# Kernel optimization log

Measured on AMD Instinct MI355X. Metric: run time of the kernel, lower is better.

## Reference

```python
import jax, jax.numpy as jnp
import numpy as np

B, H, F = 4096, 32, 1024     # batch, hp_num, feat_dim
N_CAT, CAT_DIM = 8, 16       # categorical dims 0..7, each |domain| = 16
N_CONT = H - N_CAT
LN_EPS = 1e-5


def setup_inputs() -> dict:
    key = jax.random.key(0)
    ks = jax.random.split(key, 8)
    s = 1.0 / np.sqrt(F)  # ~xavier scale
    return {
        "z": jax.random.normal(ks[0], (B, F), jnp.float32),
        "edge": jax.random.randint(ks[1], (2, 10), 0, B),
        # stacked per-hp projection Linears (weights stored as [in, out])
        "W_proj": jax.random.normal(ks[2], (H, F, F), jnp.float32) * s,
        "b_proj": jnp.zeros((H, F), jnp.float32),
        # LayerNorm over [hp_num, feat_dim]
        "ln_w": jnp.ones((H, F), jnp.float32),
        "ln_b": jnp.zeros((H, F), jnp.float32),
        # reverse_embedding for categorical dims (softmax heads)
        "W_cat": jax.random.normal(ks[3], (N_CAT, F, CAT_DIM), jnp.float32) * s,
        "b_cat": jnp.zeros((N_CAT, CAT_DIM), jnp.float32),
        # reverse_embedding for continuous dims (scalar heads)
        "W_cont": jax.random.normal(ks[4], (N_CONT, F, 1), jnp.float32) * s,
        "b_cont": jnp.zeros((N_CONT, 1), jnp.float32),
    }


def reference(z, edge, W_proj, b_proj, ln_w, ln_b, W_cat, b_cat, W_cont, b_cont):
    # per-hp projection: batched GEMM replacing batch*hp_num tiny Linears
    latent = jnp.einsum('bf,hfd->bhd', z, W_proj) + b_proj  # [B, H, F]
    # LayerNorm normalized over the last two dims [hp_num, feat_dim]
    mu = latent.mean(axis=(1, 2), keepdims=True)
    var = latent.var(axis=(1, 2), keepdims=True)
    latent = (latent - mu) * jax.lax.rsqrt(var + LN_EPS) * ln_w + ln_b
    latent = jax.nn.relu(latent)
    # reverse embeddings: categorical heads (dims 0..N_CAT-1) get softmax
    cat_logits = jnp.einsum('bhf,hfc->bhc', latent[:, :N_CAT], W_cat) + b_cat
    pred_cat = jax.nn.softmax(cat_logits, axis=-1)          # [B, N_CAT, CAT_DIM]
    pred_cont = jnp.einsum('bhf,hfc->bhc', latent[:, N_CAT:], W_cont) + b_cont  # [B, N_CONT, 1]
    return pred_cat, pred_cont, latent
```

## Files before the change

### kernel.cpp

```cpp
#include <hip/hip_runtime.h>

typedef unsigned short u16;
typedef __bf16 bf16x8 __attribute__((ext_vector_type(8)));
typedef float f32x4 __attribute__((ext_vector_type(4)));

#define B_SZ   4096
#define H_NUM  32
#define F_DIM  1024
#define NTOT   (H_NUM * F_DIM)
#define N_CAT  8
#define CAT_D  16
#define N_CONT 24
#define LN_EPS 1e-5f
#define NSTRIP 128

__device__ __forceinline__ u16 f2bf(float f) {
    unsigned int u = __builtin_bit_cast(unsigned int, f);
    unsigned int r = (u + 0x7FFFu + ((u >> 16) & 1u)) >> 16;
    return (u16)r;
}

__device__ __forceinline__ float bf2f(u16 v) {
    unsigned int u = ((unsigned int)v) << 16;
    return __builtin_bit_cast(float, u);
}

__device__ __forceinline__ void gl2lds16(const void* g, void* l) {
    __builtin_amdgcn_global_load_lds(
        (const __attribute__((address_space(1))) void*)g,
        (__attribute__((address_space(3))) void*)l,
        16, 0, 0);
}

__device__ __forceinline__ float wave_sum(float v) {
#pragma unroll
    for (int o = 32; o; o >>= 1) v += __shfl_xor(v, o);
    return v;
}

__global__ __launch_bounds__(256) void zconv(const float* __restrict__ z,
                                             u16* __restrict__ zb) {
    int i = blockIdx.x * 256 + threadIdx.x;
    float4 v = ((const float4*)z)[i];
    ushort4 o;
    o.x = f2bf(v.x); o.y = f2bf(v.y); o.z = f2bf(v.z); o.w = f2bf(v.w);
    ((ushort4*)zb)[i] = o;
}

__global__ __launch_bounds__(256) void transpose_w(const float* __restrict__ W,
                                                   u16* __restrict__ Wt) {
    __shared__ u16 tile[64][72];
    const int h = blockIdx.z;
    const int f0 = blockIdx.x * 64;
    const int d0 = blockIdx.y * 64;
    const float* Wh = W + (size_t)h * F_DIM * F_DIM;
    u16* Wth = Wt + (size_t)h * F_DIM * F_DIM;
    const int t = threadIdx.x;

#pragma unroll
    for (int i = 0; i < 4; ++i) {
        int idx = i * 256 + t;
        int fr = idx >> 4;
        int c4 = idx & 15;
        float4 v = *(const float4*)(Wh + (size_t)(f0 + fr) * F_DIM + d0 + c4 * 4);
        tile[fr][c4 * 4 + 0] = f2bf(v.x);
        tile[fr][c4 * 4 + 1] = f2bf(v.y);
        tile[fr][c4 * 4 + 2] = f2bf(v.z);
        tile[fr][c4 * 4 + 3] = f2bf(v.w);
    }
    __syncthreads();
#pragma unroll
    for (int i = 0; i < 2; ++i) {
        int idx = i * 256 + t;
        int dr = idx >> 3;
        int c8 = idx & 7;
        __attribute__((aligned(16))) u16 tmp[8];
#pragma unroll
        for (int j = 0; j < 8; ++j) tmp[j] = tile[c8 * 8 + j][dr];
        *(uint4*)(Wth + (size_t)(d0 + dr) * F_DIM + f0 + c8 * 8) = *(const uint4*)tmp;
    }
}

template <int BF>
__global__ __launch_bounds__(512, 2) void gemm256(const u16* __restrict__ A,
                                                  const u16* __restrict__ Bt,
                                                  const float* __restrict__ bproj,
                                                  u16* __restrict__ lat16,
                                                  float* __restrict__ latf,
                                                  float* __restrict__ psum,
                                                  float* __restrict__ psumsq) {
    extern __shared__ u16 dynlds[];
    const int t = threadIdx.x;
    const int wid = t >> 6;
    const int lane = t & 63;
    const int l16 = lane & 15;
    const int lk = lane >> 4;
    const int wm = wid >> 2;
    const int wn = wid & 3;

    const int wg = blockIdx.x;
    const int xcd = wg & 7;
    const int local = wg >> 3;
    const int m0 = (local & 15) * 256;
    const int n0 = ((xcd << 4) + (local >> 4)) * 256;

    f32x4 acc[8][4];
    const f32x4 zero = {0.f, 0.f, 0.f, 0.f};
#pragma unroll
    for (int m = 0; m < 8; ++m)
#pragma unroll
        for (int n = 0; n < 4; ++n) acc[m][n] = zero;

    auto stage = [&](int p, int ktn, int bn) {
        const char* srcbase = (p < 2) ? (const char*)A : (const char*)Bt;
        const int rowbase = (p < 2) ? (m0 + p * 128) : (n0 + (p - 2) * 128);
        u16* ldsbase = dynlds + bn * 32768 + (p >> 1) * 16384 + (p & 1) * 8192;
#pragma unroll
        for (int i = 0; i < 2; ++i) {
            int oo = i * 8192 + t * 16;
            int oos = oo ^ (((oo >> 7) & 7) << 4);
            int row = oo >> 7;
            int colb = oos & 127;
            gl2lds16(srcbase + (size_t)(rowbase + row) * 2048 + ktn * 128 + colb,
                     ldsbase + i * 4096 + (wid << 9));
        }
    };

#pragma unroll
    for (int p = 0; p < 4; ++p) stage(p, 0, 0);
    __syncthreads();

    const int swz = (l16 & 7) << 4;
    for (int kt = 0; kt < 16; ++kt) {
        const int buf = kt & 1;
        const char* aB = (const char*)(dynlds + buf * 32768 + wm * 8192);
        const char* bB = (const char*)(dynlds + buf * 32768 + 16384 + (wn >> 1) * 8192);
        bf16x8 bfr[4][2];
#pragma unroll
        for (int p = 0; p < 4; ++p) {
            if (kt < 15) stage(p, kt + 1, buf ^ 1);
            if (p == 0) {
#pragma unroll
                for (int nr = 0; nr < 4; ++nr)
#pragma unroll
                    for (int kk = 0; kk < 2; ++kk)
                        bfr[nr][kk] = *(const bf16x8*)(bB +
                            ((wn & 1) * 64 + nr * 16 + l16) * 128 +
                            ((kk * 64 + lk * 16) ^ swz));
            }
            bf16x8 afr[2][2];
#pragma unroll
            for (int mr = 0; mr < 2; ++mr)
#pragma unroll
                for (int kk = 0; kk < 2; ++kk)
                    afr[mr][kk] = *(const bf16x8*)(aB +
                        (p * 32 + mr * 16 + l16) * 128 +
                        ((kk * 64 + lk * 16) ^ swz));
            __builtin_amdgcn_s_setprio(1);
#pragma unroll
            for (int kk = 0; kk < 2; ++kk)
#pragma unroll
                for (int mr = 0; mr < 2; ++mr)
#pragma unroll
                    for (int nr = 0; nr < 4; ++nr)
                        acc[p * 2 + mr][nr] = __builtin_amdgcn_mfma_f32_16x16x32_bf16(
                            afr[mr][kk], bfr[nr][kk], acc[p * 2 + mr][nr], 0, 0, 0);
            __builtin_amdgcn_s_setprio(0);
        }
        __syncthreads();
    }

    float bias[4];
#pragma unroll
    for (int nr = 0; nr < 4; ++nr) bias[nr] = bproj[n0 + wn * 64 + nr * 16 + l16];

    float sm[8][4], s2[8][4];
#pragma unroll
    for (int mr = 0; mr < 8; ++mr)
#pragma unroll
        for (int j = 0; j < 4; ++j) { sm[mr][j] = 0.f; s2[mr][j] = 0.f; }

#pragma unroll
    for (int mr = 0; mr < 8; ++mr) {
#pragma unroll
        for (int j = 0; j < 4; ++j) {
            const int rowg = m0 + wm * 128 + mr * 16 + lk * 4 + j;
            size_t off = (size_t)rowg * NTOT + n0 + wn * 64 + l16;
#pragma unroll
            for (int nr = 0; nr < 4; ++nr) {
                float v = acc[mr][nr][j] + bias[nr];
                if (BF) lat16[off + nr * 16] = f2bf(v);
                else    latf[off + nr * 16] = v;
                sm[mr][j] += v;
                s2[mr][j] += v * v;
            }
        }
    }
#pragma unroll
    for (int o = 1; o < 16; o <<= 1) {
#pragma unroll
        for (int mr = 0; mr < 8; ++mr)
#pragma unroll
            for (int j = 0; j < 4; ++j) {
                sm[mr][j] += __shfl_xor(sm[mr][j], o);
                s2[mr][j] += __shfl_xor(s2[mr][j], o);
            }
    }
    float* sredf = (float*)dynlds;
    float* s2f   = sredf + 1024;
    __syncthreads();
    if (l16 == 0) {
#pragma unroll
        for (int mr = 0; mr < 8; ++mr)
#pragma unroll
            for (int j = 0; j < 4; ++j) {
                int r = wm * 128 + mr * 16 + lk * 4 + j;
                sredf[wn * 256 + r] = sm[mr][j];
                s2f[wn * 256 + r] = s2[mr][j];
            }
    }
    __syncthreads();
    if (t < 256) {
        const int strip = n0 >> 8;
        float S = sredf[t] + sredf[256 + t] + sredf[512 + t] + sredf[768 + t];
        float S2 = s2f[t] + s2f[256 + t] + s2f[512 + t] + s2f[768 + t];
        psum[(size_t)strip * B_SZ + m0 + t] = S;
        psumsq[(size_t)strip * B_SZ + m0 + t] = S2;
    }
}

__global__ __launch_bounds__(256) void ln_finalize(const float* __restrict__ psum,
                                                   const float* __restrict__ psumsq,
                                                   float* __restrict__ murs) {
    const int t = threadIdx.x;
    const int b0 = blockIdx.x * 64;
    const int tb = t & 63;
    const int tg = t >> 6;
    float s = 0.f, s2 = 0.f;
    for (int sidx = tg; sidx < NSTRIP; sidx += 4) {
        s += psum[(size_t)sidx * B_SZ + b0 + tb];
        s2 += psumsq[(size_t)sidx * B_SZ + b0 + tb];
    }
    __shared__ float r1[4][64], r2[4][64];
    r1[tg][tb] = s;
    r2[tg][tb] = s2;
    __syncthreads();
    if (t < 64) {
        float S = r1[0][t] + r1[1][t] + r1[2][t] + r1[3][t];
        float S2 = r2[0][t] + r2[1][t] + r2[2][t] + r2[3][t];
        float m = S / (float)NTOT;
        float var = S2 / (float)NTOT - m * m;
        murs[b0 + t] = m;
        murs[B_SZ + b0 + t] = rsqrtf(var + LN_EPS);
    }
}

template <int BF>
__global__ __launch_bounds__(256) void headsG(const void* __restrict__ latin_,
                                              float* __restrict__ latout,
                                              const float* __restrict__ murs,
                                              const float* __restrict__ lnw,
                                              const float* __restrict__ lnb,
                                              const float* __restrict__ Wcat,
                                              const float* __restrict__ bcat,
                                              const float* __restrict__ Wcont,
                                              const float* __restrict__ bcont,
                                              float* __restrict__ pcat,
                                              float* __restrict__ pcont) {
    const int b = blockIdx.x;
    const int t = threadIdx.x;
    const int lane = t & 63;
    const int w4 = t >> 6;
    const float mu = murs[b];
    const float rs = murs[B_SZ + b];
    const ushort4* lin16 = (const ushort4*)((const u16*)latin_ + (size_t)b * NTOT);
    const float4*  linf  = (const float4*)((const float*)latin_ + (size_t)b * NTOT);
    float4* lout4 = (float4*)(latout + (size_t)b * NTOT);
    const float4* lnw4 = (const float4*)lnw;
    const float4* lnb4 = (const float4*)lnb;
    const float4* wcont4 = (const float4*)Wcont;

    __shared__ float4 sy4[2][256];
    __shared__ float cred[4][N_CAT][CAT_D];
    __shared__ float nred[N_CONT][4];

    for (int k = 0; k < N_CAT; ++k) {
        const int i = (k << 8) + t;
        float4 x;
        if (BF) {
            ushort4 xv = lin16[i];
            x.x = bf2f(xv.x); x.y = bf2f(xv.y); x.z = bf2f(xv.z); x.w = bf2f(xv.w);
        } else {
            x = linf[i];
        }
        float4 w = lnw4[i];
        float4 bv = lnb4[i];
        float4 yo;
        yo.x = fmaxf(0.f, (x.x - mu) * rs * w.x + bv.x);
        yo.y = fmaxf(0.f, (x.y - mu) * rs * w.y + bv.y);
        yo.z = fmaxf(0.f, (x.z - mu) * rs * w.z + bv.z);
        yo.w = fmaxf(0.f, (x.w - mu) * rs * w.w + bv.w);
        lout4[i] = yo;
        sy4[k & 1][t] = yo;
        __syncthreads();

        const int c = t & 15;
        const int g = t >> 4;
        const float* Wc = Wcat + (size_t)k * F_DIM * CAT_D + c;
        float acc = 0.f;
#pragma unroll
        for (int j = 0; j < 16; ++j) {
            float4 yv = sy4[k & 1][g * 16 + j];
            int fb = (g * 64 + j * 4) * CAT_D;
            acc += yv.x * Wc[fb] + yv.y * Wc[fb + CAT_D] +
                   yv.z * Wc[fb + 2 * CAT_D] + yv.w * Wc[fb + 3 * CAT_D];
        }
        acc += __shfl_xor(acc, 16);
        acc += __shfl_xor(acc, 32);
        if (lane < 16) cred[w4][k][lane] = acc;
    }

#pragma unroll 2
    for (int k = N_CAT; k < H_NUM; ++k) {
        const int i = (k << 8) + t;
        float4 x;
        if (BF) {
            ushort4 xv = lin16[i];
            x.x = bf2f(xv.x); x.y = bf2f(xv.y); x.z = bf2f(xv.z); x.w = bf2f(xv.w);
        } else {
            x = linf[i];
        }
        float4 w = lnw4[i];
        float4 bv = lnb4[i];
        float4 wv = wcont4[((k - N_CAT) << 8) + t];
        float4 yo;
        yo.x = fmaxf(0.f, (x.x - mu) * rs * w.x + bv.x);
        yo.y = fmaxf(0.f, (x.y - mu) * rs * w.y + bv.y);
        yo.z = fmaxf(0.f, (x.z - mu) * rs * w.z + bv.z);
        yo.w = fmaxf(0.f, (x.w - mu) * rs * w.w + bv.w);
        lout4[i] = yo;
        float part = yo.x * wv.x + yo.y * wv.y + yo.z * wv.z + yo.w * wv.w;
        part = wave_sum(part);
        if (lane == 0) nred[k - N_CAT][w4] = part;
    }
    __syncthreads();

    if (t < 128) {
        const int h = t >> 4, c = t & 15;
        float lg = cred[0][h][c] + cred[1][h][c] + cred[2][h][c] + cred[3][h][c] +
                   bcat[h * CAT_D + c];
        float mx = lg;
#pragma unroll
        for (int o = 8; o; o >>= 1) mx = fmaxf(mx, __shfl_xor(mx, o, 16));
        float e = __expf(lg - mx);
        float sm2 = e;
#pragma unroll
        for (int o = 8; o; o >>= 1) sm2 += __shfl_xor(sm2, o, 16);
        pcat[(size_t)b * (N_CAT * CAT_D) + t] = e / sm2;
    } else if (t >= 128 && t < 128 + N_CONT) {
        const int ci = t - 128;
        pcont[(size_t)b * N_CONT + ci] =
            nred[ci][0] + nred[ci][1] + nred[ci][2] + nred[ci][3] + bcont[ci];
    }
}

extern "C" void kernel_launch(void* const* d_in, const int* in_sizes, int n_in,
                              void* d_out, int out_size, void* d_ws, size_t ws_size,
                              hipStream_t stream) {
    const float* z     = (const float*)d_in[0];
    const float* Wp    = (const float*)d_in[2];
    const float* bp    = (const float*)d_in[3];
    const float* lnw   = (const float*)d_in[4];
    const float* lnb   = (const float*)d_in[5];
    const float* Wcat  = (const float*)d_in[6];
    const float* bcat  = (const float*)d_in[7];
    const float* Wcont = (const float*)d_in[8];
    const float* bcont = (const float*)d_in[9];

    float* out    = (float*)d_out;
    float* pcat   = out;
    float* pcont  = out + (size_t)B_SZ * N_CAT * CAT_D;
    float* latent = pcont + (size_t)B_SZ * N_CONT;

    u16* zb     = (u16*)d_ws;
    u16* Wt     = zb + (size_t)B_SZ * F_DIM;
    float* murs = (float*)(Wt + (size_t)NTOT * F_DIM);
    float* psum   = murs + 2 * B_SZ;
    float* psumsq = psum + (size_t)B_SZ * NSTRIP;
    u16* lat16  = (u16*)(psumsq + (size_t)B_SZ * NSTRIP);

    const size_t need = (size_t)((char*)(lat16 + (size_t)B_SZ * NTOT) - (char*)d_ws);
    const bool usebf = ws_size >= need;

    const int LDSB = 131072;
    zconv<<<dim3(B_SZ * F_DIM / 1024), 256, 0, stream>>>(z, zb);
    transpose_w<<<dim3(16, 16, 32), 256, 0, stream>>>(Wp, Wt);
    if (usebf) {
        (void)hipFuncSetAttribute((const void*)gemm256<1>,
                                  hipFuncAttributeMaxDynamicSharedMemorySize, LDSB);
        gemm256<1><<<dim3(2048), 512, LDSB, stream>>>(zb, Wt, bp, lat16, nullptr,
                                                      psum, psumsq);
        ln_finalize<<<dim3(B_SZ / 64), 256, 0, stream>>>(psum, psumsq, murs);
        headsG<1><<<dim3(B_SZ), 256, 0, stream>>>(lat16, latent, murs, lnw, lnb,
                                                  Wcat, bcat, Wcont, bcont, pcat, pcont);
    } else {
        (void)hipFuncSetAttribute((const void*)gemm256<0>,
                                  hipFuncAttributeMaxDynamicSharedMemorySize, LDSB);
        gemm256<0><<<dim3(2048), 512, LDSB, stream>>>(zb, Wt, bp, nullptr, latent,
                                                      psum, psumsq);
        ln_finalize<<<dim3(B_SZ / 64), 256, 0, stream>>>(psum, psumsq, murs);
        headsG<0><<<dim3(B_SZ), 256, 0, stream>>>(latent, latent, murs, lnw, lnb,
                                                  Wcat, bcat, Wcont, bcont, pcat, pcont);
    }
}
```

Before: 761.3 us.

## Restructure heads kernel to batch categorical dots after one barrier

The heads kernel now normalizes all eight categorical feature blocks first and stores them as bf16 in shared memory, then uses a single barrier before computing all categorical dot products. Before, it synchronized once per categorical head. The continuous-head partial sums are kept in a 24-element register array and reduced after the loop, so the wave-sum shuffles are taken out of the streaming loop. The intent is fewer block barriers and more memory-level parallelism in the load/normalize phase. The cost is extra register pressure and bf16 rounding of the normalized activations feeding the softmax heads.

```diff
diff --git a/kernel.cpp b/kernel.cpp
--- a/kernel.cpp
+++ b/kernel.cpp
@@ -256,7 +256,7 @@
 }
 
 template <int BF>
-__global__ __launch_bounds__(256) void headsG(const void* __restrict__ latin_,
+__global__ __launch_bounds__(256) void headsH(const void* __restrict__ latin_,
                                               float* __restrict__ latout,
                                               const float* __restrict__ murs,
                                               const float* __restrict__ lnw,
@@ -280,10 +280,11 @@
     const float4* lnb4 = (const float4*)lnb;
     const float4* wcont4 = (const float4*)Wcont;
 
-    __shared__ float4 sy4[2][256];
+    __shared__ ushort4 sy16[N_CAT * 256];
     __shared__ float cred[4][N_CAT][CAT_D];
     __shared__ float nred[N_CONT][4];
 
+#pragma unroll 2
     for (int k = 0; k < N_CAT; ++k) {
         const int i = (k << 8) + t;
         float4 x;
@@ -301,25 +302,12 @@
         yo.z = fmaxf(0.f, (x.z - mu) * rs * w.z + bv.z);
         yo.w = fmaxf(0.f, (x.w - mu) * rs * w.w + bv.w);
         lout4[i] = yo;
-        sy4[k & 1][t] = yo;
-        __syncthreads();
-
-        const int c = t & 15;
-        const int g = t >> 4;
-        const float* Wc = Wcat + (size_t)k * F_DIM * CAT_D + c;
-        float acc = 0.f;
-#pragma unroll
-        for (int j = 0; j < 16; ++j) {
-            float4 yv = sy4[k & 1][g * 16 + j];
-            int fb = (g * 64 + j * 4) * CAT_D;
-            acc += yv.x * Wc[fb] + yv.y * Wc[fb + CAT_D] +
-                   yv.z * Wc[fb + 2 * CAT_D] + yv.w * Wc[fb + 3 * CAT_D];
-        }
-        acc += __shfl_xor(acc, 16);
-        acc += __shfl_xor(acc, 32);
-        if (lane < 16) cred[w4][k][lane] = acc;
-    }
-
+        ushort4 ys;
+        ys.x = f2bf(yo.x); ys.y = f2bf(yo.y); ys.z = f2bf(yo.z); ys.w = f2bf(yo.w);
+        sy16[i] = ys;
+    }
+
+    float cp[N_CONT];
 #pragma unroll 2
     for (int k = N_CAT; k < H_NUM; ++k) {
         const int i = (k << 8) + t;
@@ -339,16 +327,37 @@
         yo.z = fmaxf(0.f, (x.z - mu) * rs * w.z + bv.z);
         yo.w = fmaxf(0.f, (x.w - mu) * rs * w.w + bv.w);
         lout4[i] = yo;
-        float part = yo.x * wv.x + yo.y * wv.y + yo.z * wv.z + yo.w * wv.w;
-        part = wave_sum(part);
-        if (lane == 0) nred[k - N_CAT][w4] = part;
+        cp[k - N_CAT] = yo.x * wv.x + yo.y * wv.y + yo.z * wv.z + yo.w * wv.w;
+    }
+    __syncthreads();
+
+    const int c = t & 15;
+    const int g = t >> 4;
+    for (int k = 0; k < N_CAT; ++k) {
+        const float* Wc = Wcat + (size_t)k * F_DIM * CAT_D + c;
+        float acc = 0.f;
+#pragma unroll
+        for (int j = 0; j < 16; ++j) {
+            ushort4 yv = sy16[(k << 8) + g * 16 + j];
+            int fb = (g * 64 + j * 4) * CAT_D;
+            acc += bf2f(yv.x) * Wc[fb] + bf2f(yv.y) * Wc[fb + CAT_D] +
+                   bf2f(yv.z) * Wc[fb + 2 * CAT_D] + bf2f(yv.w) * Wc[fb + 3 * CAT_D];
+        }
+        acc += __shfl_xor(acc, 16);
+        acc += __shfl_xor(acc, 32);
+        if (lane < 16) cred[w4][k][lane] = acc;
+    }
+#pragma unroll
+    for (int k = 0; k < N_CONT; ++k) {
+        float v = wave_sum(cp[k]);
+        if (lane == 0) nred[k][w4] = v;
     }
     __syncthreads();
 
     if (t < 128) {
-        const int h = t >> 4, c = t & 15;
-        float lg = cred[0][h][c] + cred[1][h][c] + cred[2][h][c] + cred[3][h][c] +
-                   bcat[h * CAT_D + c];
+        const int h = t >> 4, cc = t & 15;
+        float lg = cred[0][h][cc] + cred[1][h][cc] + cred[2][h][cc] + cred[3][h][cc] +
+                   bcat[h * CAT_D + cc];
         float mx = lg;
 #pragma unroll
         for (int o = 8; o; o >>= 1) mx = fmaxf(mx, __shfl_xor(mx, o, 16));
@@ -401,7 +410,7 @@
         gemm256<1><<<dim3(2048), 512, LDSB, stream>>>(zb, Wt, bp, lat16, nullptr,
                                                       psum, psumsq);
         ln_finalize<<<dim3(B_SZ / 64), 256, 0, stream>>>(psum, psumsq, murs);
-        headsG<1><<<dim3(B_SZ), 256, 0, stream>>>(lat16, latent, murs, lnw, lnb,
+        headsH<1><<<dim3(B_SZ), 256, 0, stream>>>(lat16, latent, murs, lnw, lnb,
                                                   Wcat, bcat, Wcont, bcont, pcat, pcont);
     } else {
         (void)hipFuncSetAttribute((const void*)gemm256<0>,
@@ -409,7 +418,7 @@
         gemm256<0><<<dim3(2048), 512, LDSB, stream>>>(zb, Wt, bp, nullptr, latent,
                                                       psum, psumsq);
         ln_finalize<<<dim3(B_SZ / 64), 256, 0, stream>>>(psum, psumsq, murs);
-        headsG<0><<<dim3(B_SZ), 256, 0, stream>>>(latent, latent, murs, lnw, lnb,
+        headsH<0><<<dim3(B_SZ), 256, 0, stream>>>(latent, latent, murs, lnw, lnb,
                                                   Wcat, bcat, Wcont, bcont, pcat, pcont);
     }
 }
```

New measurement: 745.7 us. -2.1%, faster.
